# Kernel optimization log

Hardware: AMD Instinct MI355X
Metric: run time of the kernel (lower is better)

The kernel has to match this reference:

```python
import jax, jax.numpy as jnp
import numpy as np

B, K, P = 16, 64, 256
D_MODEL, EXPAND = 512, 2
D_INNER = D_MODEL * EXPAND  # 1024
D_CONV, D_FF, E_LAYERS = 4, 16, 4
DT_RANK = 32  # ceil(512/16)
RANK = 4


def rmsnorm(x, w, eps=1e-5):
    return x * jax.lax.rsqrt(jnp.mean(x * x, axis=-1, keepdims=True) + eps) * w


def selective_scan(u, delta, A, Bm, Cm, Dp):
    # u,delta: [b,l,d]; A: [d,n]; Bm,Cm: [b,l,n]; Dp: [d]
    dA = jnp.exp(jnp.einsum('bld,dn->bldn', delta, A))
    dBu = jnp.einsum('bld,bln,bld->bldn', delta, Bm, u)
    x0 = jnp.zeros((u.shape[0], u.shape[2], A.shape[1]), u.dtype)

    def step(x, t):
        dA_t, dBu_t, c_t = t
        x = dA_t * x + dBu_t
        return x, jnp.einsum('bdn,bn->bd', x, c_t)

    _, ys = jax.lax.scan(step, x0, (dA.swapaxes(0, 1), dBu.swapaxes(0, 1), Cm.swapaxes(0, 1)))
    return ys.swapaxes(0, 1) + u * Dp


def mamba_block(h, in_w, cw, cb, xp_w, dt_w, dt_b, A_log, Dp, out_w):
    b, l, _ = h.shape
    xr = h @ in_w.T  # [b,l,2*d_inner]
    x, res = xr[..., :D_INNER], xr[..., D_INNER:]
    # causal depthwise conv1d (torch pads d_conv-1 both sides then trims to l)
    xc = jax.lax.conv_general_dilated(
        x.swapaxes(1, 2), cw, (1,), [(D_CONV - 1, 0)],
        feature_group_count=D_INNER, dimension_numbers=('NCH', 'OIH', 'NCH'))
    x = jax.nn.silu((xc + cb[:, None]).swapaxes(1, 2))
    A = -jnp.exp(A_log)
    x_dbl = x @ xp_w.T
    delta = jax.nn.softplus(x_dbl[..., :DT_RANK] @ dt_w.T + dt_b)
    Bm = x_dbl[..., DT_RANK:DT_RANK + D_FF]
    Cm = x_dbl[..., DT_RANK + D_FF:]
    y = selective_scan(x, delta, A, Bm, Cm, Dp)
    y = y * jax.nn.silu(res)
    return y @ out_w.T


def setup_inputs() -> dict:
    key = jax.random.key(0)
    ks = iter(jax.random.split(key, 32))
    rn = lambda s, sc=0.02: jax.random.normal(next(ks), s, jnp.float32) * sc
    A_init = jnp.log(jnp.tile(jnp.arange(1, D_FF + 1, dtype=jnp.float32)[None, None, :],
                              (E_LAYERS, D_INNER, 1)))
    return {
        'inputs': jax.random.normal(next(ks), (B, K, P), jnp.float32),
        'sp_lin1_w': rn((D_MODEL, P)), 'sp_lin1_b': jnp.zeros((D_MODEL,)),
        'sp_lin2_w': rn((D_MODEL, D_MODEL)), 'sp_lin2_b': jnp.zeros((D_MODEL,)),
        'sp_gate_w': rn((D_MODEL, P)), 'sp_gate_b': jnp.zeros((D_MODEL,)),
        'sp_norm_w': jnp.ones((D_MODEL,)),
        'in_proj_w': rn((E_LAYERS, 2 * D_INNER, D_MODEL)),
        'conv_w': rn((E_LAYERS, D_INNER, 1, D_CONV)),
        'conv_b': jnp.zeros((E_LAYERS, D_INNER)),
        'x_proj_w': rn((E_LAYERS, DT_RANK + 2 * D_FF, D_INNER)),
        'dt_proj_w': rn((E_LAYERS, D_INNER, DT_RANK)),
        'dt_proj_b': jnp.zeros((E_LAYERS, D_INNER)),
        'A_log': A_init,
        'D': jnp.ones((E_LAYERS, D_INNER)),
        'out_proj_w': rn((E_LAYERS, D_MODEL, D_INNER)),
        'blk_norm_w': jnp.ones((E_LAYERS, D_MODEL)),
        'post_norm_w': jnp.ones((D_MODEL,)),
        'proj_w': rn((2 * P * RANK, D_MODEL)),
    }


def reference(inputs, sp_lin1_w, sp_lin1_b, sp_lin2_w, sp_lin2_b, sp_gate_w, sp_gate_b,
              sp_norm_w, in_proj_w, conv_w, conv_b, x_proj_w, dt_proj_w, dt_proj_b,
              A_log, D, out_proj_w, blk_norm_w, post_norm_w, proj_w):
    # SpatialEncoder, shared across lags (pure last-dim linears -> apply to [B,K,P])
    h = jax.nn.gelu(inputs @ sp_lin1_w.T + sp_lin1_b, approximate=False)
    h = h @ sp_lin2_w.T + sp_lin2_b
    g = jax.nn.sigmoid(inputs @ sp_gate_w.T + sp_gate_b)
    h = rmsnorm(h * g, sp_norm_w)  # [B,K,d_model]
    for l in range(E_LAYERS):
        h = mamba_block(rmsnorm(h, blk_norm_w[l]), in_proj_w[l], conv_w[l], conv_b[l],
                        x_proj_w[l], dt_proj_w[l], dt_proj_b[l], A_log[l], D[l],
                        out_proj_w[l]) + h
    h = rmsnorm(h, post_norm_w)
    out = h @ proj_w.T  # [B,K,2*P*RANK]
    U = out[..., :P * RANK].reshape(B, K, P, RANK)
    V = out[..., P * RANK:].reshape(B, K, P, RANK)
    coeffs = jnp.einsum('bkpr,bkqr->bkpq', U, V)
    preds = jnp.einsum('bkpq,bkq->bp', coeffs, inputs)
    return preds, coeffs
```

## Files before the change

### kernel.cpp

```cpp
#include <hip/hip_runtime.h>
#include <hip/hip_bf16.h>
#include <math.h>

namespace {

constexpr int SEQ    = 64;
constexpr int DINNER = 1024;
constexpr int DFF    = 16;
constexpr int DTRANK = 32;
constexpr int WXPD_STRIDE = 1056 * 1024;

typedef __attribute__((ext_vector_type(8))) short short8;
typedef __attribute__((ext_vector_type(4))) float f32x4;
typedef __attribute__((address_space(3))) unsigned int lds_u32_t;
typedef __attribute__((address_space(1))) unsigned int glb_u32_t;

__device__ __forceinline__ float sigm(float x) { return 1.f / (1.f + __expf(-x)); }
__device__ __forceinline__ short f2b(float v) {
    __hip_bfloat16 h = __float2bfloat16(v);
    return *(short*)&h;
}
__device__ __forceinline__ float b2f(short s) {
    union { unsigned u; float f; } c; c.u = ((unsigned)(unsigned short)s) << 16; return c.f;
}
__device__ __forceinline__ float softp(float v) {
    return fmaxf(v, 0.f) + log1pf(__expf(-fabsf(v)));
}

__device__ __forceinline__ void gemm_core64(
    f32x4 (&acc)[2][2],
    const short* __restrict__ A, int lda,
    const short* __restrict__ W, int ldw,
    int Kd, short* As, short* Bs, int m0, int n0)
{
    constexpr int SZ = 64 * 32;
    const int tid = threadIdx.x, wave = tid >> 6, lane = tid & 63;
    const int wm = wave >> 1, wn = wave & 1;
    const int l15 = lane & 15, kg = lane >> 4;

    const int p = wave * 64 + lane;
    const short* srcA = A + (size_t)(m0 + (p >> 2)) * lda + (p & 3) * 8;
    const short* srcB = W + (size_t)(n0 + (p >> 2)) * ldw + (p & 3) * 8;
    const int ob = (wave * 64) * 8;

    const int nt = Kd >> 5;
    __builtin_amdgcn_global_load_lds((const glb_u32_t*)srcA, (lds_u32_t*)(As + ob), 16, 0, 0);
    __builtin_amdgcn_global_load_lds((const glb_u32_t*)srcB, (lds_u32_t*)(Bs + ob), 16, 0, 0);

    for (int t = 0; t < nt; t++) {
        __syncthreads();
        if (t + 1 < nt) {
            const int k0 = (t + 1) * 32;
            const int s = ((t + 1) & 1) * SZ;
            __builtin_amdgcn_global_load_lds((const glb_u32_t*)(srcA + k0), (lds_u32_t*)(As + s + ob), 16, 0, 0);
            __builtin_amdgcn_global_load_lds((const glb_u32_t*)(srcB + k0), (lds_u32_t*)(Bs + s + ob), 16, 0, 0);
        }
        const short* Ab = As + (t & 1) * SZ;
        const short* Bb = Bs + (t & 1) * SZ;
        short8 af[2], bfr[2];
#pragma unroll
        for (int mi = 0; mi < 2; mi++)
            af[mi] = *(const short8*)(Ab + (wm * 32 + mi * 16 + l15) * 32 + kg * 8);
#pragma unroll
        for (int ni = 0; ni < 2; ni++)
            bfr[ni] = *(const short8*)(Bb + (wn * 32 + ni * 16 + l15) * 32 + kg * 8);
#pragma unroll
        for (int mi = 0; mi < 2; mi++)
#pragma unroll
            for (int ni = 0; ni < 2; ni++)
                acc[mi][ni] = __builtin_amdgcn_mfma_f32_16x16x32_bf16(af[mi], bfr[ni], acc[mi][ni], 0, 0, 0);
    }
}

__global__ __launch_bounds__(256) void prep_k(
    const float* __restrict__ lin1_w, const float* __restrict__ gate_w,
    const float* __restrict__ lin2_w, const float* __restrict__ in_proj_w,
    const float* __restrict__ out_proj_w, const float* __restrict__ proj_w,
    const float* __restrict__ x_proj_w, const float* __restrict__ dt_proj_w,
    const float* __restrict__ inputs, const float* __restrict__ blk_norm_w,
    const float* __restrict__ post_norm_w,
    short* __restrict__ wlin1gb, short* __restrict__ wlin2b, short* __restrict__ winpb,
    short* __restrict__ woutpb, short* __restrict__ wprojb, short* __restrict__ wxpdb,
    short* __restrict__ inputsb, float* __restrict__ preds, float* __restrict__ ss)
{
    const int blk = blockIdx.x, tid = threadIdx.x;
    if (blk < 1024) {
        const int wave = tid >> 6, lane = tid & 63;
        const int nrow = blk * 4 + wave;
        const int l = nrow >> 10, n = nrow & 1023;
        const float* dtw = dt_proj_w + (size_t)l * 32768 + n * 32;
        const float* xpw = x_proj_w + (size_t)l * 65536;
        float4 acc[4] = {};
        for (int r = 0; r < 32; r++) {
            const float s = dtw[r];
#pragma unroll
            for (int rep = 0; rep < 4; rep++) {
                const float4 xv = *(const float4*)(xpw + r * 1024 + rep * 256 + lane * 4);
                acc[rep].x = fmaf(s, xv.x, acc[rep].x);
                acc[rep].y = fmaf(s, xv.y, acc[rep].y);
                acc[rep].z = fmaf(s, xv.z, acc[rep].z);
                acc[rep].w = fmaf(s, xv.w, acc[rep].w);
            }
        }
        short* dst = wxpdb + (size_t)l * WXPD_STRIDE + (size_t)(32 + n) * 1024;
#pragma unroll
        for (int rep = 0; rep < 4; rep++) {
            union { short sh[4]; uint2 u; } pk;
            pk.sh[0] = f2b(acc[rep].x); pk.sh[1] = f2b(acc[rep].y);
            pk.sh[2] = f2b(acc[rep].z); pk.sh[3] = f2b(acc[rep].w);
            *(uint2*)(dst + rep * 256 + lane * 4) = pk.u;
        }
    } else if (blk < 1056) {
#pragma unroll
        for (int rep = 0; rep < 4; rep++) {
            const int idx = (blk - 1024) * 4096 + rep * 1024 + tid * 4;
            const int l = idx >> 15, off = idx & 32767;
            const float4 v = *(const float4*)(x_proj_w + (size_t)l * 65536 + 32768 + off);
            union { short sh[4]; uint2 u; } pk;
            pk.sh[0] = f2b(v.x); pk.sh[1] = f2b(v.y); pk.sh[2] = f2b(v.z); pk.sh[3] = f2b(v.w);
            *(uint2*)(wxpdb + (size_t)l * WXPD_STRIDE + off) = pk.u;
        }
    } else if (blk < 2016) {
        constexpr int pre[8] = {0, 128, 256, 512, 4608, 6656, 7680, 7936};
        for (int vb = blk - 1056; vb < 7936; vb += 960) {
            int s = 0;
#pragma unroll
            for (int i = 1; i < 7; i++) s += (vb >= pre[i]);
            const int e = (vb - pre[s]) * 1024 + tid * 4;
            const float* src; short* dst;
            bool hasG = false; const float* gp = nullptr;
            if      (s == 0) { src = lin1_w + e;     dst = wlin1gb + e; }
            else if (s == 1) { src = gate_w + e;     dst = wlin1gb + 131072 + e; }
            else if (s == 2) { src = lin2_w + e;     dst = wlin2b + e; }
            else if (s == 3) { src = in_proj_w + e;  dst = winpb + e;
                               hasG = true; gp = blk_norm_w + (e >> 20) * 512 + (e & 511); }
            else if (s == 4) { src = out_proj_w + e; dst = woutpb + e; }
            else if (s == 5) { src = proj_w + e;     dst = wprojb + e;
                               hasG = true; gp = post_norm_w + (e & 511); }
            else             { src = inputs + e;     dst = inputsb + e; }
            float4 v = *(const float4*)src;
            if (hasG) {
                const float4 gv = *(const float4*)gp;
                v.x *= gv.x; v.y *= gv.y; v.z *= gv.z; v.w *= gv.w;
            }
            union { short sh[4]; uint2 u; } pk;
            pk.sh[0] = f2b(v.x); pk.sh[1] = f2b(v.y); pk.sh[2] = f2b(v.z); pk.sh[3] = f2b(v.w);
            *(uint2*)dst = pk.u;
        }
    } else {
        const int i = (blk - 2016) * 256 + tid;
        if (i < 4096) preds[i] = 0.f;
        else ss[1024 + (i - 4096)] = 0.f;
    }
}

__global__ __launch_bounds__(256) void lin1gate_k(
    const short* __restrict__ A, const short* __restrict__ W,
    const float* __restrict__ b1, const float* __restrict__ b2,
    short* __restrict__ h1b, float* __restrict__ g)
{
    __shared__ short As[2 * 64 * 32];
    __shared__ short Bs[2 * 64 * 32];
    f32x4 acc[2][2] = {};
    const int m0 = blockIdx.y * 64, n0 = blockIdx.x * 64;
    gemm_core64(acc, A, 256, W, 256, 256, As, Bs, m0, n0);
    const int lane = threadIdx.x & 63, wave = threadIdx.x >> 6;
    const int wm = wave >> 1, wn = wave & 1, l15 = lane & 15, kg = lane >> 4;
#pragma unroll
    for (int ni = 0; ni < 2; ni++) {
        const int col = n0 + wn * 32 + ni * 16 + l15;
        const bool isG = col >= 512;
        const float b = isG ? b2[col - 512] : b1[col];
#pragma unroll
        for (int mi = 0; mi < 2; mi++)
#pragma unroll
            for (int j = 0; j < 4; j++) {
                const int row = m0 + wm * 32 + mi * 16 + kg * 4 + j;
                const float v = acc[mi][ni][j] + b;
                if (isG) g[(size_t)row * 512 + (col - 512)] = sigm(v);
                else     h1b[(size_t)row * 512 + col] = f2b(0.5f * v * (1.f + erff(v * 0.70710678f)));
            }
    }
}

__global__ __launch_bounds__(256) void lin2_k(
    const short* __restrict__ A, const short* __restrict__ W,
    const float* __restrict__ bias, const float* __restrict__ g, float* __restrict__ x)
{
    __shared__ short As[2 * 64 * 32];
    __shared__ short Bs[2 * 64 * 32];
    f32x4 acc[2][2] = {};
    const int m0 = blockIdx.y * 64, n0 = blockIdx.x * 64;
    gemm_core64(acc, A, 512, W, 512, 512, As, Bs, m0, n0);
    const int lane = threadIdx.x & 63, wave = threadIdx.x >> 6;
    const int wm = wave >> 1, wn = wave & 1, l15 = lane & 15, kg = lane >> 4;
#pragma unroll
    for (int ni = 0; ni < 2; ni++) {
        const int col = n0 + wn * 32 + ni * 16 + l15;
        const float b = bias[col];
#pragma unroll
        for (int mi = 0; mi < 2; mi++)
#pragma unroll
            for (int j = 0; j < 4; j++) {
                const int row = m0 + wm * 32 + mi * 16 + kg * 4 + j;
                x[(size_t)row * 512 + col] = (acc[mi][ni][j] + b) * g[(size_t)row * 512 + col];
            }
    }
}

__global__ __launch_bounds__(256) void rms_sp_k(
    const float* __restrict__ x, const float* __restrict__ w,
    float* __restrict__ h, short* __restrict__ hb, float* __restrict__ ss0)
{
    const int lane = threadIdx.x & 63;
    const int rowId = blockIdx.x * 4 + (threadIdx.x >> 6);
    const float* ip = x + (size_t)rowId * 512 + lane * 8;
    const float4 v1 = *(const float4*)ip;
    const float4 v2 = *(const float4*)(ip + 4);
    float sq = v1.x * v1.x + v1.y * v1.y + v1.z * v1.z + v1.w * v1.w
             + v2.x * v2.x + v2.y * v2.y + v2.z * v2.z + v2.w * v2.w;
#pragma unroll
    for (int off = 32; off > 0; off >>= 1) sq += __shfl_xor(sq, off, 64);
    const float rs = rsqrtf(sq * (1.f / 512.f) + 1e-5f);
    const float4 w1 = *(const float4*)(w + lane * 8);
    const float4 w2 = *(const float4*)(w + lane * 8 + 4);
    const float o[8] = { v1.x * rs * w1.x, v1.y * rs * w1.y, v1.z * rs * w1.z, v1.w * rs * w1.w,
                         v2.x * rs * w2.x, v2.y * rs * w2.y, v2.z * rs * w2.z, v2.w * rs * w2.w };
    float* op = h + (size_t)rowId * 512 + lane * 8;
    *(float4*)op       = make_float4(o[0], o[1], o[2], o[3]);
    *(float4*)(op + 4) = make_float4(o[4], o[5], o[6], o[7]);
    short8 pk;
#pragma unroll
    for (int i = 0; i < 8; i++) pk[i] = f2b(o[i]);
    *(short8*)(hb + (size_t)rowId * 512 + lane * 8) = pk;
    float s2 = 0.f;
#pragma unroll
    for (int i = 0; i < 8; i++) s2 = fmaf(o[i], o[i], s2);
#pragma unroll
    for (int off = 32; off > 0; off >>= 1) s2 += __shfl_xor(s2, off, 64);
    if (lane == 0) ss0[rowId] = s2;
}

union ConvU {
    struct { short As[2 * 64 * 32]; short Bs[2 * 64 * 32]; } gm;
    float cbuf[67][68];
};

__global__ __launch_bounds__(256) void inprojconv_k(
    const short* __restrict__ A, const short* __restrict__ W,
    const float* __restrict__ ss_in, const float* __restrict__ cw,
    const float* __restrict__ cb, short* __restrict__ xcb, short* __restrict__ srb)
{
    __shared__ ConvU u;
    f32x4 acc[2][2] = {};
    const int m0 = blockIdx.y * 64, n0 = blockIdx.x * 64;
    gemm_core64(acc, A, 512, W, 512, 512, u.gm.As, u.gm.Bs, m0, n0);
    const int tid = threadIdx.x;
    const int lane = tid & 63, wave = tid >> 6;
    const int wm = wave >> 1, wn = wave & 1, l15 = lane & 15, kg = lane >> 4;

#pragma unroll
    for (int mi = 0; mi < 2; mi++)
#pragma unroll
        for (int j = 0; j < 4; j++) {
            const int row = m0 + wm * 32 + mi * 16 + kg * 4 + j;
            const float r = rsqrtf(ss_in[row] * (1.f / 512.f) + 1e-5f);
#pragma unroll
            for (int ni = 0; ni < 2; ni++) acc[mi][ni][j] *= r;
        }

    if (n0 < 1024) {
        const int ccol = tid & 63;
        const int rg = tid >> 6;
        const int d = n0 + ccol;
        const float4 w4 = *(const float4*)(cw + d * 4);
        const float bia = cb[d];

        __syncthreads();
#pragma unroll
        for (int mi = 0; mi < 2; mi++)
#pragma unroll
            for (int ni = 0; ni < 2; ni++)
#pragma unroll
                for (int j = 0; j < 4; j++)
                    u.cbuf[3 + wm * 32 + mi * 16 + kg * 4 + j][wn * 32 + ni * 16 + l15] = acc[mi][ni][j];
        for (int i = tid; i < 3 * 68; i += 256) u.cbuf[i / 68][i % 68] = 0.f;
        __syncthreads();
#pragma unroll 4
        for (int k = 0; k < 16; k++) {
            const int row = rg + 4 * k;
            float v = bia + w4.x * u.cbuf[row][ccol] + w4.y * u.cbuf[row + 1][ccol]
                          + w4.z * u.cbuf[row + 2][ccol] + w4.w * u.cbuf[row + 3][ccol];
            v = v * sigm(v);
            xcb[(size_t)(m0 + row) * 1024 + d] = f2b(v);
        }
    } else {
#pragma unroll
        for (int ni = 0; ni < 2; ni++) {
            const int scol = n0 - 1024 + wn * 32 + ni * 16 + l15;
#pragma unroll
            for (int mi = 0; mi < 2; mi++)
#pragma unroll
                for (int j = 0; j < 4; j++) {
                    const int row = m0 + wm * 32 + mi * 16 + kg * 4 + j;
                    const float v = acc[mi][ni][j];
                    srb[(size_t)row * 1024 + scol] = f2b(v * sigm(v));
                }
        }
    }
}

union XsU {
    struct { short As[2 * 64 * 32]; short Wd[2 * 64 * 32]; short BC[2 * 32 * 32]; } gm;
    struct { float dlt[64][68]; float BC[64][32]; } sc;
};

__global__ __launch_bounds__(256) void xpdscan_k(
    const short* __restrict__ A , const short* __restrict__ W ,
    const float* __restrict__ dtb, const float* __restrict__ Alog,
    const float* __restrict__ Dp, const short* __restrict__ srb, short* __restrict__ yb)
{
    __shared__ XsU u;
    const int dg = blockIdx.x, b = blockIdx.y;
    const int m0 = b * 64;
    const int tid = threadIdx.x;
    const int lane = tid & 63, wave = tid >> 6;
    const int wm = wave >> 1, wn = wave & 1, l15 = lane & 15, kg = lane >> 4;

    constexpr int SZA = 64 * 32, SZBC = 32 * 32;
    const int p = wave * 64 + lane;
    const short* srcA  = A + (size_t)(m0 + (p >> 2)) * 1024 + (p & 3) * 8;
    const short* srcWd = W + (size_t)(32 + dg * 64 + (p >> 2)) * 1024 + (p & 3) * 8;
    const short* srcBC = W + (size_t)(p >> 2) * 1024 + (p & 3) * 8;
    const int ob = (wave * 64) * 8;

    f32x4 accd[2][2] = {};
    f32x4 accx[2] = {};

    __builtin_amdgcn_global_load_lds((const glb_u32_t*)srcA,  (lds_u32_t*)(u.gm.As + ob), 16, 0, 0);
    __builtin_amdgcn_global_load_lds((const glb_u32_t*)srcWd, (lds_u32_t*)(u.gm.Wd + ob), 16, 0, 0);
    if (wave < 2)
        __builtin_amdgcn_global_load_lds((const glb_u32_t*)srcBC, (lds_u32_t*)(u.gm.BC + ob), 16, 0, 0);

    for (int t = 0; t < 32; t++) {
        __syncthreads();
        if (t + 1 < 32) {
            const int k0 = (t + 1) * 32;
            const int sA = ((t + 1) & 1) * SZA, sBC = ((t + 1) & 1) * SZBC;
            __builtin_amdgcn_global_load_lds((const glb_u32_t*)(srcA + k0),  (lds_u32_t*)(u.gm.As + sA + ob), 16, 0, 0);
            __builtin_amdgcn_global_load_lds((const glb_u32_t*)(srcWd + k0), (lds_u32_t*)(u.gm.Wd + sA + ob), 16, 0, 0);
            if (wave < 2)
                __builtin_amdgcn_global_load_lds((const glb_u32_t*)(srcBC + k0), (lds_u32_t*)(u.gm.BC + sBC + ob), 16, 0, 0);
        }
        const short* Ab  = u.gm.As + (t & 1) * SZA;
        const short* Wdb = u.gm.Wd + (t & 1) * SZA;
        const short* BCb = u.gm.BC + (t & 1) * SZBC;
        short8 af[2], wf[2], bcf;
#pragma unroll
        for (int mi = 0; mi < 2; mi++)
            af[mi] = *(const short8*)(Ab + (wm * 32 + mi * 16 + l15) * 32 + kg * 8);
#pragma unroll
        for (int ni = 0; ni < 2; ni++)
            wf[ni] = *(const short8*)(Wdb + (wn * 32 + ni * 16 + l15) * 32 + kg * 8);
        bcf = *(const short8*)(BCb + (wn * 16 + l15) * 32 + kg * 8);
#pragma unroll
        for (int mi = 0; mi < 2; mi++) {
#pragma unroll
            for (int ni = 0; ni < 2; ni++)
                accd[mi][ni] = __builtin_amdgcn_mfma_f32_16x16x32_bf16(af[mi], wf[ni], accd[mi][ni], 0, 0, 0);
            accx[mi] = __builtin_amdgcn_mfma_f32_16x16x32_bf16(af[mi], bcf, accx[mi], 0, 0, 0);
        }
    }

    __syncthreads();
#pragma unroll
    for (int ni = 0; ni < 2; ni++) {
        const int dl = wn * 32 + ni * 16 + l15;
        const float bb = dtb[dg * 64 + dl];
#pragma unroll
        for (int mi = 0; mi < 2; mi++)
#pragma unroll
            for (int j = 0; j < 4; j++)
                u.sc.dlt[wm * 32 + mi * 16 + kg * 4 + j][dl] = softp(accd[mi][ni][j] + bb);
    }
    {
        const int c = wn * 16 + l15;
#pragma unroll
        for (int mi = 0; mi < 2; mi++)
#pragma unroll
            for (int j = 0; j < 4; j++)
                u.sc.BC[wm * 32 + mi * 16 + kg * 4 + j][c] = accx[mi][j];
    }
    __syncthreads();

    if (tid < 64) {
        const int d = dg * 64 + tid;
        float a[16], s[16];
#pragma unroll
        for (int n = 0; n < 16; n++) { a[n] = -__expf(Alog[(size_t)d * 16 + n]); s[n] = 0.f; }
        const float dv = Dp[d];
        const size_t base = (size_t)b * SEQ;
        float uu = b2f(A[base * DINNER + d]);
        float rr = b2f(srb[base * 1024 + d]);
        for (int l = 0; l < SEQ; l++) {
            float uu_n = 0.f, rr_n = 0.f;
            if (l + 1 < SEQ) {
                uu_n = b2f(A[(base + l + 1) * DINNER + d]);
                rr_n = b2f(srb[(base + l + 1) * 1024 + d]);
            }
            const float dlt = u.sc.dlt[l][tid];
            const float dbu = dlt * uu;
            float acc = 0.f;
#pragma unroll
            for (int n = 0; n < 16; n++) {
                s[n] = __expf(dlt * a[n]) * s[n] + dbu * u.sc.BC[l][n];
                acc = fmaf(s[n], u.sc.BC[l][16 + n], acc);
            }
            acc = fmaf(uu, dv, acc);
            yb[(base + l) * DINNER + d] = f2b(acc * rr);
            uu = uu_n; rr = rr_n;
        }
    }
}

__global__ __launch_bounds__(256) void outproj_k(
    const short* __restrict__ A, const short* __restrict__ W,
    float* __restrict__ h, short* __restrict__ hb, float* __restrict__ ss_out)
{
    __shared__ short As[2 * 32 * 32];
    __shared__ short Bs[2 * 64 * 32];
    constexpr int SZA = 32 * 32, SZB = 64 * 32;
    const int m0 = blockIdx.y * 32, n0 = blockIdx.x * 64;
    const int tid = threadIdx.x, wave = tid >> 6, lane = tid & 63;
    const int l15 = lane & 15, kg = lane >> 4;

    const int p = wave * 64 + lane;
    const short* srcA = A + (size_t)(m0 + (p >> 2)) * 1024 + (p & 3) * 8;
    const short* srcB = W + (size_t)(n0 + (p >> 2)) * 1024 + (p & 3) * 8;
    const int ob = (wave * 64) * 8;

    f32x4 acc[2] = {};
    if (wave < 2)
        __builtin_amdgcn_global_load_lds((const glb_u32_t*)srcA, (lds_u32_t*)(As + ob), 16, 0, 0);
    __builtin_amdgcn_global_load_lds((const glb_u32_t*)srcB, (lds_u32_t*)(Bs + ob), 16, 0, 0);

    for (int t = 0; t < 32; t++) {
        __syncthreads();
        if (t + 1 < 32) {
            const int k0 = (t + 1) * 32;
            const int sA = ((t + 1) & 1) * SZA, sB = ((t + 1) & 1) * SZB;
            if (wave < 2)
                __builtin_amdgcn_global_load_lds((const glb_u32_t*)(srcA + k0), (lds_u32_t*)(As + sA + ob), 16, 0, 0);
            __builtin_amdgcn_global_load_lds((const glb_u32_t*)(srcB + k0), (lds_u32_t*)(Bs + sB + ob), 16, 0, 0);
        }
        const short* Ab = As + (t & 1) * SZA;
        const short* Bb = Bs + (t & 1) * SZB;
        short8 af[2], bf;
#pragma unroll
        for (int mi = 0; mi < 2; mi++)
            af[mi] = *(const short8*)(Ab + (mi * 16 + l15) * 32 + kg * 8);
        bf = *(const short8*)(Bb + (wave * 16 + l15) * 32 + kg * 8);
#pragma unroll
        for (int mi = 0; mi < 2; mi++)
            acc[mi] = __builtin_amdgcn_mfma_f32_16x16x32_bf16(af[mi], bf, acc[mi], 0, 0, 0);
    }

    const int col = n0 + wave * 16 + l15;
    float vsq[2][4] = {};
#pragma unroll
    for (int mi = 0; mi < 2; mi++)
#pragma unroll
        for (int j = 0; j < 4; j++) {
            const int row = m0 + mi * 16 + kg * 4 + j;
            const float v = acc[mi][j] + h[(size_t)row * 512 + col];
            h[(size_t)row * 512 + col] = v;
            hb[(size_t)row * 512 + col] = f2b(v);
            vsq[mi][j] = v * v;
        }
#pragma unroll
    for (int mi = 0; mi < 2; mi++)
#pragma unroll
        for (int j = 0; j < 4; j++) {
            float t = vsq[mi][j];
            t += __shfl_xor(t, 1, 64);
            t += __shfl_xor(t, 2, 64);
            t += __shfl_xor(t, 4, 64);
            t += __shfl_xor(t, 8, 64);
            if (l15 == 0) {
                const int row = m0 + mi * 16 + kg * 4 + j;
                atomicAdd(ss_out + row, t);
            }
        }
}

__global__ __launch_bounds__(256) void projf_k(
    const short* __restrict__ A, const short* __restrict__ W,
    const float* __restrict__ ss_in, float* __restrict__ xr)
{
    __shared__ short As[2 * 64 * 32];
    __shared__ short Bs[2 * 64 * 32];
    f32x4 acc[2][2] = {};
    const int m0 = blockIdx.y * 64, n0 = blockIdx.x * 64;
    gemm_core64(acc, A, 512, W, 512, 512, As, Bs, m0, n0);
    const int lane = threadIdx.x & 63, wave = threadIdx.x >> 6;
    const int wm = wave >> 1, wn = wave & 1, l15 = lane & 15, kg = lane >> 4;
#pragma unroll
    for (int mi = 0; mi < 2; mi++)
#pragma unroll
        for (int j = 0; j < 4; j++) {
            const int row = m0 + wm * 32 + mi * 16 + kg * 4 + j;
            const float r = rsqrtf(ss_in[row] * (1.f / 512.f) + 1e-5f);
#pragma unroll
            for (int ni = 0; ni < 2; ni++) {
                const int col = n0 + wn * 32 + ni * 16 + l15;
                xr[(size_t)row * 2048 + col] = acc[mi][ni][j] * r;
            }
        }
}

__global__ __launch_bounds__(256) void coeffs_k(
    const float* __restrict__ outp, const float* __restrict__ inp,
    float* __restrict__ coeffs, float* __restrict__ preds)
{
    const int m = blockIdx.x;
    const int b = m >> 6;
    const int tid = threadIdx.x, wave = tid >> 6, lane = tid & 63;
    __shared__ float4 Us[256], Vs[256];
    __shared__ float ins[256];
    __shared__ float4 tpart[4];
    Us[tid] = *(const float4*)(outp + (size_t)m * 2048 + tid * 4);
    Vs[tid] = *(const float4*)(outp + (size_t)m * 2048 + 1024 + tid * 4);
    ins[tid] = inp[(size_t)m * 256 + tid];
    __syncthreads();
    const float4 vq0 = Vs[lane * 4 + 0], vq1 = Vs[lane * 4 + 1];
    const float4 vq2 = Vs[lane * 4 + 2], vq3 = Vs[lane * 4 + 3];
    float* cbase = coeffs + (size_t)m * 65536 + lane * 4;
#pragma unroll 4
    for (int i = 0; i < 64; i++) {
        const int pp = (wave << 6) + i;
        const float4 up = Us[pp];
        float4 c;
        c.x = up.x * vq0.x + up.y * vq0.y + up.z * vq0.z + up.w * vq0.w;
        c.y = up.x * vq1.x + up.y * vq1.y + up.z * vq1.z + up.w * vq1.w;
        c.z = up.x * vq2.x + up.y * vq2.y + up.z * vq2.z + up.w * vq2.w;
        c.w = up.x * vq3.x + up.y * vq3.y + up.z * vq3.z + up.w * vq3.w;
        *(float4*)(cbase + (size_t)pp * 256) = c;
    }
    const float iv = ins[tid];
    const float4 vm = Vs[tid];
    float4 t = make_float4(vm.x * iv, vm.y * iv, vm.z * iv, vm.w * iv);
#pragma unroll
    for (int off = 32; off > 0; off >>= 1) {
        t.x += __shfl_xor(t.x, off, 64);
        t.y += __shfl_xor(t.y, off, 64);
        t.z += __shfl_xor(t.z, off, 64);
        t.w += __shfl_xor(t.w, off, 64);
    }
    if (lane == 0) tpart[wave] = t;
    __syncthreads();
    const float4 t0 = tpart[0], t1 = tpart[1], t2 = tpart[2], t3 = tpart[3];
    const float4 tt = make_float4(t0.x + t1.x + t2.x + t3.x, t0.y + t1.y + t2.y + t3.y,
                                  t0.z + t1.z + t2.z + t3.z, t0.w + t1.w + t2.w + t3.w);
    const float4 up = Us[tid];
    const float pv = up.x * tt.x + up.y * tt.y + up.z * tt.z + up.w * tt.w;
    atomicAdd(preds + (size_t)b * 256 + tid, pv);
}

}

extern "C" void kernel_launch(void* const* d_in, const int* in_sizes, int n_in,
                              void* d_out, int out_size, void* d_ws, size_t ws_size,
                              hipStream_t stream)
{
    const float* inputs     = (const float*)d_in[0];
    const float* lin1_w     = (const float*)d_in[1];
    const float* lin1_b     = (const float*)d_in[2];
    const float* lin2_w     = (const float*)d_in[3];
    const float* lin2_b     = (const float*)d_in[4];
    const float* gate_w     = (const float*)d_in[5];
    const float* gate_b     = (const float*)d_in[6];
    const float* sp_norm_w  = (const float*)d_in[7];
    const float* in_proj_w  = (const float*)d_in[8];
    const float* conv_w     = (const float*)d_in[9];
    const float* conv_b     = (const float*)d_in[10];
    const float* x_proj_w   = (const float*)d_in[11];
    const float* dt_proj_w  = (const float*)d_in[12];
    const float* dt_proj_b  = (const float*)d_in[13];
    const float* A_log      = (const float*)d_in[14];
    const float* Dvec       = (const float*)d_in[15];
    const float* out_proj_w = (const float*)d_in[16];
    const float* blk_norm_w = (const float*)d_in[17];
    const float* post_norm_w= (const float*)d_in[18];
    const float* proj_w     = (const float*)d_in[19];

    float* ws = (float*)d_ws;
    float* h     = ws;
    float* xr    = ws + 524288;
    float* x     = ws + 2621440;
    float* g     = ws + 3145728;
    float* ss    = ws + 3670016;
    short* bfb     = (short*)(ws + 3676160);
    short* inputsb = bfb;
    short* h1b     = bfb + 262144;
    short* hb      = bfb + 786432;
    short* xcb     = bfb + 1310720;
    short* yb      = bfb + 2359296;
    short* srb     = bfb + 3407872;
    short* wlin1gb = bfb + 4456448;
    short* wlin2b  = bfb + 4718592;
    short* winpb   = bfb + 4980736;
    short* woutpb  = bfb + 9175040;
    short* wprojb  = bfb + 11272192;
    short* wxpdb   = bfb + 12320768;
    float* preds  = (float*)d_out;
    float* coeffs = (float*)d_out + 4096;

    const dim3 blk(256);

    prep_k<<<dim3(2048), blk, 0, stream>>>(
        lin1_w, gate_w, lin2_w, in_proj_w, out_proj_w, proj_w, x_proj_w, dt_proj_w,
        inputs, blk_norm_w, post_norm_w,
        wlin1gb, wlin2b, winpb, woutpb, wprojb, wxpdb, inputsb, preds, ss);

    lin1gate_k<<<dim3(16, 16), blk, 0, stream>>>(inputsb, wlin1gb, lin1_b, gate_b, h1b, g);
    lin2_k<<<dim3(8, 16), blk, 0, stream>>>(h1b, wlin2b, lin2_b, g, x);
    rms_sp_k<<<dim3(256), blk, 0, stream>>>(x, sp_norm_w, h, hb, ss);

    for (int l = 0; l < 4; l++) {
        inprojconv_k<<<dim3(32, 16), blk, 0, stream>>>(
            hb, winpb + (size_t)l * 1048576, ss + l * 1024,
            conv_w + (size_t)l * 4096, conv_b + l * 1024, xcb, srb);
        xpdscan_k<<<dim3(16, 16), blk, 0, stream>>>(
            xcb, wxpdb + (size_t)l * WXPD_STRIDE, dt_proj_b + l * 1024,
            A_log + (size_t)l * 16384, Dvec + l * 1024, srb, yb);
        outproj_k<<<dim3(8, 32), blk, 0, stream>>>(yb, woutpb + (size_t)l * 524288,
                                                   h, hb, ss + (l + 1) * 1024);
    }

    projf_k<<<dim3(32, 16), blk, 0, stream>>>(hb, wprojb, ss + 4096, xr);
    coeffs_k<<<dim3(1024), blk, 0, stream>>>(xr, inputs, coeffs, preds);
}
```

Before: 414.1 us.

## Fuse spatial RMSNorm into lin2 epilogue and parallelize scan across state dims

Removes the separate spatial RMSNorm kernel. lin2 now writes the pre-norm activations plus two row sum-of-squares via atomics. The first layer's in_proj folds the sp_norm weight into its bf16 weights and applies a combined double-rsqrt scale, and the first out_proj rebuilds the normalized residual from the raw activations. Separately, the selective scan now uses all 256 threads, four per channel with four states each, reduced by shuffles, instead of 64 threads each running 16 states. prep_k also computes two dt_proj rows per wave, giving fewer blocks. The costs are extra atomics, templated kernel variants, and reuse of the yb buffer for the bf16 activations.

```diff
diff --git a/kernel.cpp b/kernel.cpp
--- a/kernel.cpp
+++ b/kernel.cpp
@@ -6,8 +6,6 @@
 
 constexpr int SEQ    = 64;
 constexpr int DINNER = 1024;
-constexpr int DFF    = 16;
-constexpr int DTRANK = 32;
 constexpr int WXPD_STRIDE = 1056 * 1024;
 
 typedef __attribute__((ext_vector_type(8))) short short8;
@@ -78,62 +76,69 @@
     const float* __restrict__ out_proj_w, const float* __restrict__ proj_w,
     const float* __restrict__ x_proj_w, const float* __restrict__ dt_proj_w,
     const float* __restrict__ inputs, const float* __restrict__ blk_norm_w,
-    const float* __restrict__ post_norm_w,
+    const float* __restrict__ post_norm_w, const float* __restrict__ sp_norm_w,
     short* __restrict__ wlin1gb, short* __restrict__ wlin2b, short* __restrict__ winpb,
     short* __restrict__ woutpb, short* __restrict__ wprojb, short* __restrict__ wxpdb,
     short* __restrict__ inputsb, float* __restrict__ preds, float* __restrict__ ss)
 {
     const int blk = blockIdx.x, tid = threadIdx.x;
-    if (blk < 1024) {
+    if (blk < 512) {
         const int wave = tid >> 6, lane = tid & 63;
-        const int nrow = blk * 4 + wave;
+        const int nrow = blk * 8 + wave * 2;
         const int l = nrow >> 10, n = nrow & 1023;
-        const float* dtw = dt_proj_w + (size_t)l * 32768 + n * 32;
+        const float* dtw0 = dt_proj_w + (size_t)l * 32768 + n * 32;
+        const float* dtw1 = dtw0 + 32;
         const float* xpw = x_proj_w + (size_t)l * 65536;
-        float4 acc[4] = {};
+        float4 a0[4] = {}, a1[4] = {};
         for (int r = 0; r < 32; r++) {
-            const float s = dtw[r];
+            const float s0 = dtw0[r], s1 = dtw1[r];
 #pragma unroll
             for (int rep = 0; rep < 4; rep++) {
                 const float4 xv = *(const float4*)(xpw + r * 1024 + rep * 256 + lane * 4);
-                acc[rep].x = fmaf(s, xv.x, acc[rep].x);
-                acc[rep].y = fmaf(s, xv.y, acc[rep].y);
-                acc[rep].z = fmaf(s, xv.z, acc[rep].z);
-                acc[rep].w = fmaf(s, xv.w, acc[rep].w);
-            }
-        }
-        short* dst = wxpdb + (size_t)l * WXPD_STRIDE + (size_t)(32 + n) * 1024;
+                a0[rep].x = fmaf(s0, xv.x, a0[rep].x); a0[rep].y = fmaf(s0, xv.y, a0[rep].y);
+                a0[rep].z = fmaf(s0, xv.z, a0[rep].z); a0[rep].w = fmaf(s0, xv.w, a0[rep].w);
+                a1[rep].x = fmaf(s1, xv.x, a1[rep].x); a1[rep].y = fmaf(s1, xv.y, a1[rep].y);
+                a1[rep].z = fmaf(s1, xv.z, a1[rep].z); a1[rep].w = fmaf(s1, xv.w, a1[rep].w);
+            }
+        }
+        short* dst0 = wxpdb + (size_t)l * WXPD_STRIDE + (size_t)(32 + n) * 1024;
+        short* dst1 = dst0 + 1024;
 #pragma unroll
         for (int rep = 0; rep < 4; rep++) {
-            union { short sh[4]; uint2 u; } pk;
-            pk.sh[0] = f2b(acc[rep].x); pk.sh[1] = f2b(acc[rep].y);
-            pk.sh[2] = f2b(acc[rep].z); pk.sh[3] = f2b(acc[rep].w);
-            *(uint2*)(dst + rep * 256 + lane * 4) = pk.u;
-        }
-    } else if (blk < 1056) {
+            union { short sh[4]; uint2 u; } p0, p1;
+            p0.sh[0] = f2b(a0[rep].x); p0.sh[1] = f2b(a0[rep].y);
+            p0.sh[2] = f2b(a0[rep].z); p0.sh[3] = f2b(a0[rep].w);
+            p1.sh[0] = f2b(a1[rep].x); p1.sh[1] = f2b(a1[rep].y);
+            p1.sh[2] = f2b(a1[rep].z); p1.sh[3] = f2b(a1[rep].w);
+            *(uint2*)(dst0 + rep * 256 + lane * 4) = p0.u;
+            *(uint2*)(dst1 + rep * 256 + lane * 4) = p1.u;
+        }
+    } else if (blk < 544) {
 #pragma unroll
         for (int rep = 0; rep < 4; rep++) {
-            const int idx = (blk - 1024) * 4096 + rep * 1024 + tid * 4;
+            const int idx = (blk - 512) * 4096 + rep * 1024 + tid * 4;
             const int l = idx >> 15, off = idx & 32767;
             const float4 v = *(const float4*)(x_proj_w + (size_t)l * 65536 + 32768 + off);
             union { short sh[4]; uint2 u; } pk;
             pk.sh[0] = f2b(v.x); pk.sh[1] = f2b(v.y); pk.sh[2] = f2b(v.z); pk.sh[3] = f2b(v.w);
             *(uint2*)(wxpdb + (size_t)l * WXPD_STRIDE + off) = pk.u;
         }
-    } else if (blk < 2016) {
+    } else if (blk < 1504) {
         constexpr int pre[8] = {0, 128, 256, 512, 4608, 6656, 7680, 7936};
-        for (int vb = blk - 1056; vb < 7936; vb += 960) {
+        for (int vb = blk - 544; vb < 7936; vb += 960) {
             int s = 0;
 #pragma unroll
             for (int i = 1; i < 7; i++) s += (vb >= pre[i]);
             const int e = (vb - pre[s]) * 1024 + tid * 4;
             const float* src; short* dst;
             bool hasG = false; const float* gp = nullptr;
+            bool hasSp = false;
             if      (s == 0) { src = lin1_w + e;     dst = wlin1gb + e; }
             else if (s == 1) { src = gate_w + e;     dst = wlin1gb + 131072 + e; }
             else if (s == 2) { src = lin2_w + e;     dst = wlin2b + e; }
             else if (s == 3) { src = in_proj_w + e;  dst = winpb + e;
-                               hasG = true; gp = blk_norm_w + (e >> 20) * 512 + (e & 511); }
+                               hasG = true; gp = blk_norm_w + (e >> 20) * 512 + (e & 511);
+                               hasSp = ((e >> 20) == 0); }
             else if (s == 4) { src = out_proj_w + e; dst = woutpb + e; }
             else if (s == 5) { src = proj_w + e;     dst = wprojb + e;
                                hasG = true; gp = post_norm_w + (e & 511); }
@@ -143,14 +148,18 @@
                 const float4 gv = *(const float4*)gp;
                 v.x *= gv.x; v.y *= gv.y; v.z *= gv.z; v.w *= gv.w;
             }
+            if (hasSp) {
+                const float4 sv = *(const float4*)(sp_norm_w + (e & 511));
+                v.x *= sv.x; v.y *= sv.y; v.z *= sv.z; v.w *= sv.w;
+            }
             union { short sh[4]; uint2 u; } pk;
             pk.sh[0] = f2b(v.x); pk.sh[1] = f2b(v.y); pk.sh[2] = f2b(v.z); pk.sh[3] = f2b(v.w);
             *(uint2*)dst = pk.u;
         }
     } else {
-        const int i = (blk - 2016) * 256 + tid;
+        const int i = (blk - 1504) * 256 + tid;
         if (i < 4096) preds[i] = 0.f;
-        else ss[1024 + (i - 4096)] = 0.f;
+        else ss[i - 4096] = 0.f;
     }
 }
 
@@ -185,7 +194,9 @@
 
 __global__ __launch_bounds__(256) void lin2_k(
     const short* __restrict__ A, const short* __restrict__ W,
-    const float* __restrict__ bias, const float* __restrict__ g, float* __restrict__ x)
+    const float* __restrict__ bias, const float* __restrict__ g,
+    const float* __restrict__ gsp, float* __restrict__ x, short* __restrict__ xb,
+    float* __restrict__ ssS1, float* __restrict__ ssS2)
 {
     __shared__ short As[2 * 64 * 32];
     __shared__ short Bs[2 * 64 * 32];
@@ -194,51 +205,40 @@
     gemm_core64(acc, A, 512, W, 512, 512, As, Bs, m0, n0);
     const int lane = threadIdx.x & 63, wave = threadIdx.x >> 6;
     const int wm = wave >> 1, wn = wave & 1, l15 = lane & 15, kg = lane >> 4;
+    float vs1[2][4] = {}, vs2[2][4] = {};
 #pragma unroll
     for (int ni = 0; ni < 2; ni++) {
         const int col = n0 + wn * 32 + ni * 16 + l15;
         const float b = bias[col];
+        const float gc = gsp[col];
 #pragma unroll
         for (int mi = 0; mi < 2; mi++)
 #pragma unroll
             for (int j = 0; j < 4; j++) {
                 const int row = m0 + wm * 32 + mi * 16 + kg * 4 + j;
-                x[(size_t)row * 512 + col] = (acc[mi][ni][j] + b) * g[(size_t)row * 512 + col];
-            }
-    }
-}
-
-__global__ __launch_bounds__(256) void rms_sp_k(
-    const float* __restrict__ x, const float* __restrict__ w,
-    float* __restrict__ h, short* __restrict__ hb, float* __restrict__ ss0)
-{
-    const int lane = threadIdx.x & 63;
-    const int rowId = blockIdx.x * 4 + (threadIdx.x >> 6);
-    const float* ip = x + (size_t)rowId * 512 + lane * 8;
-    const float4 v1 = *(const float4*)ip;
-    const float4 v2 = *(const float4*)(ip + 4);
-    float sq = v1.x * v1.x + v1.y * v1.y + v1.z * v1.z + v1.w * v1.w
-             + v2.x * v2.x + v2.y * v2.y + v2.z * v2.z + v2.w * v2.w;
-#pragma unroll
-    for (int off = 32; off > 0; off >>= 1) sq += __shfl_xor(sq, off, 64);
-    const float rs = rsqrtf(sq * (1.f / 512.f) + 1e-5f);
-    const float4 w1 = *(const float4*)(w + lane * 8);
-    const float4 w2 = *(const float4*)(w + lane * 8 + 4);
-    const float o[8] = { v1.x * rs * w1.x, v1.y * rs * w1.y, v1.z * rs * w1.z, v1.w * rs * w1.w,
-                         v2.x * rs * w2.x, v2.y * rs * w2.y, v2.z * rs * w2.z, v2.w * rs * w2.w };
-    float* op = h + (size_t)rowId * 512 + lane * 8;
-    *(float4*)op       = make_float4(o[0], o[1], o[2], o[3]);
-    *(float4*)(op + 4) = make_float4(o[4], o[5], o[6], o[7]);
-    short8 pk;
-#pragma unroll
-    for (int i = 0; i < 8; i++) pk[i] = f2b(o[i]);
-    *(short8*)(hb + (size_t)rowId * 512 + lane * 8) = pk;
-    float s2 = 0.f;
-#pragma unroll
-    for (int i = 0; i < 8; i++) s2 = fmaf(o[i], o[i], s2);
-#pragma unroll
-    for (int off = 32; off > 0; off >>= 1) s2 += __shfl_xor(s2, off, 64);
-    if (lane == 0) ss0[rowId] = s2;
+                const float v = (acc[mi][ni][j] + b) * g[(size_t)row * 512 + col];
+                x[(size_t)row * 512 + col] = v;
+                xb[(size_t)row * 512 + col] = f2b(v);
+                vs1[mi][j] = fmaf(v, v, vs1[mi][j]);
+                const float w = v * gc;
+                vs2[mi][j] = fmaf(w, w, vs2[mi][j]);
+            }
+    }
+#pragma unroll
+    for (int mi = 0; mi < 2; mi++)
+#pragma unroll
+        for (int j = 0; j < 4; j++) {
+            float t1 = vs1[mi][j], t2 = vs2[mi][j];
+            t1 += __shfl_xor(t1, 1, 64); t2 += __shfl_xor(t2, 1, 64);
+            t1 += __shfl_xor(t1, 2, 64); t2 += __shfl_xor(t2, 2, 64);
+            t1 += __shfl_xor(t1, 4, 64); t2 += __shfl_xor(t2, 4, 64);
+            t1 += __shfl_xor(t1, 8, 64); t2 += __shfl_xor(t2, 8, 64);
+            if (l15 == 0) {
+                const int row = m0 + wm * 32 + mi * 16 + kg * 4 + j;
+                atomicAdd(ssS1 + row, t1);
+                atomicAdd(ssS2 + row, t2);
+            }
+        }
 }
 
 union ConvU {
@@ -246,10 +246,12 @@
     float cbuf[67][68];
 };
 
+template <int COMB>
 __global__ __launch_bounds__(256) void inprojconv_k(
     const short* __restrict__ A, const short* __restrict__ W,
-    const float* __restrict__ ss_in, const float* __restrict__ cw,
-    const float* __restrict__ cb, short* __restrict__ xcb, short* __restrict__ srb)
+    const float* __restrict__ ssA, const float* __restrict__ ssB,
+    const float* __restrict__ cw, const float* __restrict__ cb,
+    short* __restrict__ xcb, short* __restrict__ srb)
 {
     __shared__ ConvU u;
     f32x4 acc[2][2] = {};
@@ -264,7 +266,13 @@
 #pragma unroll
         for (int j = 0; j < 4; j++) {
             const int row = m0 + wm * 32 + mi * 16 + kg * 4 + j;
-            const float r = rsqrtf(ss_in[row] * (1.f / 512.f) + 1e-5f);
+            float r;
+            if constexpr (COMB) {
+                const float rx = rsqrtf(ssA[row] * (1.f / 512.f) + 1e-5f);
+                r = rx * rsqrtf(rx * rx * ssB[row] * (1.f / 512.f) + 1e-5f);
+            } else {
+                r = rsqrtf(ssA[row] * (1.f / 512.f) + 1e-5f);
+            }
 #pragma unroll
             for (int ni = 0; ni < 2; ni++) acc[mi][ni][j] *= r;
         }
@@ -393,11 +401,16 @@
     }
     __syncthreads();
 
-    if (tid < 64) {
-        const int d = dg * 64 + tid;
-        float a[16], s[16];
-#pragma unroll
-        for (int n = 0; n < 16; n++) { a[n] = -__expf(Alog[(size_t)d * 16 + n]); s[n] = 0.f; }
+    {
+        const int d_l = tid >> 2;
+        const int ns = (tid & 3) << 2;
+        const int d = dg * 64 + d_l;
+        float a[4], s[4];
+#pragma unroll
+        for (int n = 0; n < 4; n++) {
+            a[n] = -__expf(Alog[(size_t)d * 16 + ns + n]);
+            s[n] = 0.f;
+        }
         const float dv = Dp[d];
         const size_t base = (size_t)b * SEQ;
         float uu = b2f(A[base * DINNER + d]);
@@ -408,24 +421,29 @@
                 uu_n = b2f(A[(base + l + 1) * DINNER + d]);
                 rr_n = b2f(srb[(base + l + 1) * 1024 + d]);
             }
-            const float dlt = u.sc.dlt[l][tid];
+            const float dlt = u.sc.dlt[l][d_l];
             const float dbu = dlt * uu;
-            float acc = 0.f;
-#pragma unroll
-            for (int n = 0; n < 16; n++) {
-                s[n] = __expf(dlt * a[n]) * s[n] + dbu * u.sc.BC[l][n];
-                acc = fmaf(s[n], u.sc.BC[l][16 + n], acc);
-            }
-            acc = fmaf(uu, dv, acc);
-            yb[(base + l) * DINNER + d] = f2b(acc * rr);
+            float part = 0.f;
+#pragma unroll
+            for (int n = 0; n < 4; n++) {
+                s[n] = __expf(dlt * a[n]) * s[n] + dbu * u.sc.BC[l][ns + n];
+                part = fmaf(s[n], u.sc.BC[l][16 + ns + n], part);
+            }
+            part += __shfl_xor(part, 1, 64);
+            part += __shfl_xor(part, 2, 64);
+            if ((tid & 3) == 0)
+                yb[(base + l) * DINNER + d] = f2b((part + uu * dv) * rr);
             uu = uu_n; rr = rr_n;
         }
     }
 }
 
+template <int FIRST>
 __global__ __launch_bounds__(256) void outproj_k(
     const short* __restrict__ A, const short* __restrict__ W,
-    float* __restrict__ h, short* __restrict__ hb, float* __restrict__ ss_out)
+    float* __restrict__ h, short* __restrict__ hb, float* __restrict__ ss_out,
+    const float* __restrict__ xsrc, const float* __restrict__ gsp,
+    const float* __restrict__ ssS1)
 {
     __shared__ short As[2 * 32 * 32];
     __shared__ short Bs[2 * 64 * 32];
@@ -466,13 +484,21 @@
     }
 
     const int col = n0 + wave * 16 + l15;
+    const float gc = FIRST ? gsp[col] : 0.f;
     float vsq[2][4] = {};
 #pragma unroll
     for (int mi = 0; mi < 2; mi++)
 #pragma unroll
         for (int j = 0; j < 4; j++) {
             const int row = m0 + mi * 16 + kg * 4 + j;
-            const float v = acc[mi][j] + h[(size_t)row * 512 + col];
+            float hold;
+            if constexpr (FIRST) {
+                const float rx = rsqrtf(ssS1[row] * (1.f / 512.f) + 1e-5f);
+                hold = xsrc[(size_t)row * 512 + col] * rx * gc;
+            } else {
+                hold = h[(size_t)row * 512 + col];
+            }
+            const float v = acc[mi][j] + hold;
             h[(size_t)row * 512 + col] = v;
             hb[(size_t)row * 512 + col] = f2b(v);
             vsq[mi][j] = v * v;
@@ -605,6 +631,7 @@
     short* hb      = bfb + 786432;
     short* xcb     = bfb + 1310720;
     short* yb      = bfb + 2359296;
+    short* xb      = yb;
     short* srb     = bfb + 3407872;
     short* wlin1gb = bfb + 4456448;
     short* wlin2b  = bfb + 4718592;
@@ -617,24 +644,33 @@
 
     const dim3 blk(256);
 
-    prep_k<<<dim3(2048), blk, 0, stream>>>(
+    prep_k<<<dim3(1544), blk, 0, stream>>>(
         lin1_w, gate_w, lin2_w, in_proj_w, out_proj_w, proj_w, x_proj_w, dt_proj_w,
-        inputs, blk_norm_w, post_norm_w,
+        inputs, blk_norm_w, post_norm_w, sp_norm_w,
         wlin1gb, wlin2b, winpb, woutpb, wprojb, wxpdb, inputsb, preds, ss);
 
     lin1gate_k<<<dim3(16, 16), blk, 0, stream>>>(inputsb, wlin1gb, lin1_b, gate_b, h1b, g);
-    lin2_k<<<dim3(8, 16), blk, 0, stream>>>(h1b, wlin2b, lin2_b, g, x);
-    rms_sp_k<<<dim3(256), blk, 0, stream>>>(x, sp_norm_w, h, hb, ss);
+    lin2_k<<<dim3(8, 16), blk, 0, stream>>>(h1b, wlin2b, lin2_b, g, sp_norm_w,
+                                            x, xb, ss, ss + 5120);
 
     for (int l = 0; l < 4; l++) {
-        inprojconv_k<<<dim3(32, 16), blk, 0, stream>>>(
-            hb, winpb + (size_t)l * 1048576, ss + l * 1024,
-            conv_w + (size_t)l * 4096, conv_b + l * 1024, xcb, srb);
+        if (l == 0)
+            inprojconv_k<1><<<dim3(32, 16), blk, 0, stream>>>(
+                xb, winpb, ss, ss + 5120,
+                conv_w, conv_b, xcb, srb);
+        else
+            inprojconv_k<0><<<dim3(32, 16), blk, 0, stream>>>(
+                hb, winpb + (size_t)l * 1048576, ss + l * 1024, nullptr,
+                conv_w + (size_t)l * 4096, conv_b + l * 1024, xcb, srb);
         xpdscan_k<<<dim3(16, 16), blk, 0, stream>>>(
             xcb, wxpdb + (size_t)l * WXPD_STRIDE, dt_proj_b + l * 1024,
             A_log + (size_t)l * 16384, Dvec + l * 1024, srb, yb);
-        outproj_k<<<dim3(8, 32), blk, 0, stream>>>(yb, woutpb + (size_t)l * 524288,
-                                                   h, hb, ss + (l + 1) * 1024);
+        if (l == 0)
+            outproj_k<1><<<dim3(8, 32), blk, 0, stream>>>(yb, woutpb,
+                h, hb, ss + 1024, x, sp_norm_w, ss);
+        else
+            outproj_k<0><<<dim3(8, 32), blk, 0, stream>>>(yb, woutpb + (size_t)l * 524288,
+                h, hb, ss + (l + 1) * 1024, nullptr, nullptr, nullptr);
     }
 
     projf_k<<<dim3(32, 16), blk, 0, stream>>>(hb, wprojb, ss + 4096, xr);
```

Result: faster. 404.0 us (-2.5%).
